# Kernel optimization log

Measured on AMD Instinct MI355X. Metric: run time of the kernel, lower is better.

Reference implementation:

```python
import jax, jax.numpy as jnp
import numpy as np

FFT_SIZE = 1024
HOP = 256

def _dft_weights(fft_size):
    # Matches torch module: np.fft.fft(np.eye(N)) * np.hanning(N)
    # fft_mat[k, n] = exp(-2j*pi*k*n/N) * hanning[n]
    fft_mat = np.fft.fft(np.eye(fft_size)) * np.hanning(fft_size)
    real_w = jnp.asarray(np.real(fft_mat), dtype=jnp.float32)  # [N, N]
    imag_w = jnp.asarray(np.imag(fft_mat), dtype=jnp.float32)  # [N, N]
    return real_w, imag_w

def setup_inputs() -> dict:
    key = jax.random.key(0)
    x = jax.random.normal(key, (32, 160000), dtype=jnp.float32)
    real_w, imag_w = _dft_weights(FFT_SIZE)
    return {"x": x, "real_w": real_w, "imag_w": imag_w}

def reference(x, real_w, imag_w):
    N = FFT_SIZE
    hop = HOP
    B, L = x.shape
    n_frames = (L - N) // hop + 1
    # Frame extraction: frames[b, t, n] = x[b, t*hop + n]
    idx = jnp.arange(n_frames)[:, None] * hop + jnp.arange(N)[None, :]  # [T, N]
    frames = x[:, idx]  # [B, T, N]
    # DFT-as-GEMM (same math as Conv1d(1, N, N, stride=hop) with DFT weights)
    real_x = jnp.einsum('btn,kn->bkt', frames, real_w)  # [B, N, T]
    imag_x = jnp.einsum('btn,kn->bkt', frames, imag_w)  # [B, N, T]
    mag = (real_x ** 2 + imag_x ** 2)[:, :N // 2 + 1, :]  # [B, N//2+1, T]
    phase = jnp.arctan2(imag_x, real_x)  # [B, N, T]
    return (mag, phase)
```

## Files before the change

### kernel.cpp

```cpp
#include <hip/hip_runtime.h>
#include <math.h>

#define NFFT     1024
#define HOP      256
#define NFRAMES  622
#define NBATCH   32
#define XLEN     160000
#define TILE_T   16
#define NPAIR    8
#define ROW      1234
#define KBINS    513
#define NT       512
#define NTILES   39
#define NBLK     (NTILES*NBATCH)

#define PAD(i)   ((i) + 2*((i)>>4) + 4*((i)>>6) + 8*((i)>>8))

#define C1 0.9238795325112867f
#define S1 0.3826834323650898f
#define C2 0.7071067811865476f

__device__ __forceinline__ float2 cmul(float2 a, float2 b) {
    return make_float2(a.x*b.x - a.y*b.y, a.x*b.y + a.y*b.x);
}
__device__ __forceinline__ float2 csqr(float2 a) {
    return make_float2(a.x*a.x - a.y*a.y, 2.0f*a.x*a.y);
}

__device__ __forceinline__ float2 w_of_rev(float f) {
    float s, c;
    asm("v_sin_f32 %0, %1" : "=v"(s) : "v"(f));
    asm("v_cos_f32 %0, %1" : "=v"(c) : "v"(f));
    return make_float2(c, s);
}

__device__ __forceinline__ void bfly4(float2& a, float2& b, float2& c, float2& d,
                                      float2 w1, float2 w2, float2 w3) {
    float2 apc = make_float2(a.x + c.x, a.y + c.y);
    float2 amc = make_float2(a.x - c.x, a.y - c.y);
    float2 bpd = make_float2(b.x + d.x, b.y + d.y);
    float2 bmd = make_float2(b.x - d.x, b.y - d.y);
    float2 y0 = make_float2(apc.x + bpd.x, apc.y + bpd.y);
    float2 y2 = make_float2(apc.x - bpd.x, apc.y - bpd.y);
    float2 y1 = make_float2(amc.x + bmd.y, amc.y - bmd.x);
    float2 y3 = make_float2(amc.x - bmd.y, amc.y + bmd.x);
    a = y0; b = cmul(w1, y1); c = cmul(w2, y2); d = cmul(w3, y3);
}
__device__ __forceinline__ void bfly4_nw(float2& a, float2& b, float2& c, float2& d) {
    float2 apc = make_float2(a.x + c.x, a.y + c.y);
    float2 amc = make_float2(a.x - c.x, a.y - c.y);
    float2 bpd = make_float2(b.x + d.x, b.y + d.y);
    float2 bmd = make_float2(b.x - d.x, b.y - d.y);
    a = make_float2(apc.x + bpd.x, apc.y + bpd.y);
    b = make_float2(amc.x + bmd.y, amc.y - bmd.x);
    c = make_float2(apc.x - bpd.x, apc.y - bpd.y);
    d = make_float2(amc.x - bmd.y, amc.y + bmd.x);
}

__device__ __forceinline__ void fence() {
    asm volatile("s_waitcnt lgkmcnt(0)" ::: "memory");
    __builtin_amdgcn_sched_barrier(0);
}

__device__ __forceinline__ float fast_atan2f(float y, float x) {
    const float ax = fabsf(x), ay = fabsf(y);
    const float mx = fmaxf(ax, ay), mn = fminf(ax, ay);
    float r = mn * __builtin_amdgcn_rcpf(mx);
    if (mx == 0.0f) r = 0.0f;
    const float t = r * r;
    float p = fmaf(t, -0.01172120f, 0.05265332f);
    p = fmaf(t, p, -0.11643287f);
    p = fmaf(t, p, 0.19354346f);
    p = fmaf(t, p, -0.33262347f);
    p = fmaf(t, p, 0.99997726f);
    float a = r * p;
    a = (ay > ax) ? (1.5707963267948966f - a) : a;
    a = (x < 0.0f) ? (3.14159265358979323f - a) : a;
    return copysignf(a, y);
}

__global__ __launch_bounds__(NT, 4)
void spec_kernel(const float* __restrict__ x, const float* __restrict__ win,
                 float* __restrict__ out)
{
    __shared__ __align__(16) float2 zb[NPAIR * ROW];

    const int tid = threadIdx.x;
    const int lg  = (blockIdx.x & 7) * (NBLK / 8) + (blockIdx.x >> 3);
    const int b   = lg / NTILES;
    const int t0  = (lg - b * NTILES) * TILE_T;
    const int wv  = tid >> 6;
    const int ln  = tid & 63;

    {
        const int f0 = t0 + 2*wv, f1 = f0 + 1;
        const float* xb = x + (size_t)b * XLEN;
        const bool v0 = (f0 < NFRAMES), v1 = (f1 < NFRAMES);
        float4* D4 = reinterpret_cast<float4*>(
            &zb[wv*ROW + 4*ln + 2*(ln>>2) + 4*(ln>>4)]);
        #pragma unroll
        for (int q = 0; q < 4; ++q) {
            const int n0 = (q << 8) + (ln << 2);
            const float4 w4 = *reinterpret_cast<const float4*>(&win[n0]);
            float4 a4 = make_float4(0.f, 0.f, 0.f, 0.f), b4 = a4;
            if (v0) a4 = *reinterpret_cast<const float4*>(&xb[f0*HOP + n0]);
            if (v1) b4 = *reinterpret_cast<const float4*>(&xb[f1*HOP + n0]);
            D4[156*q]     = make_float4(w4.x*a4.x, w4.x*b4.x, w4.y*a4.y, w4.y*b4.y);
            D4[156*q + 1] = make_float4(w4.z*a4.z, w4.z*b4.z, w4.w*a4.w, w4.w*b4.w);
        }
    }
    fence();

    {
        float2* p = &zb[wv*ROW + ln + 2*(ln>>4)];
        float2 E[16];
        #pragma unroll
        for (int j = 0; j < 16; ++j) E[j] = p[76*j + 8*(j>>2)];
        const float2 wc = w_of_rev((float)ln * (-1.0f/1024.0f));
        #pragma unroll
        for (int q = 0; q < 4; ++q) {
            float2 w1;
            if      (q == 0) w1 = wc;
            else if (q == 1) w1 = cmul(wc, make_float2(C1, -S1));
            else if (q == 2) w1 = cmul(wc, make_float2(C2, -C2));
            else             w1 = cmul(wc, make_float2(S1, -C1));
            float2 w2 = csqr(w1), w3 = cmul(w1, w2);
            bfly4(E[q], E[q+4], E[q+8], E[q+12], w1, w2, w3);
        }
        const float2 wb  = w_of_rev((float)ln * (-4.0f/1024.0f));
        const float2 wb2 = csqr(wb), wb3 = cmul(wb, wb2);
        #pragma unroll
        for (int u = 0; u < 4; ++u)
            bfly4(E[4*u], E[4*u+1], E[4*u+2], E[4*u+3], wb, wb2, wb3);
        #pragma unroll
        for (int j = 0; j < 16; ++j) p[76*j + 8*(j>>2)] = E[j];
    }
    fence();

    {
        const int m = ln & 15, h = ln >> 4;
        float2* p = &zb[wv*ROW + 76*h + m];
        const float2 w1 = w_of_rev((float)m * (-1.0f/64.0f));
        const float2 w2 = csqr(w1), w3 = cmul(w1, w2);
        #pragma unroll
        for (int u = 0; u < 4; ++u) {
            float2 a  = p[312*u],      bb = p[312*u + 18];
            float2 cc = p[312*u + 36], dd = p[312*u + 54];
            bfly4(a, bb, cc, dd, w1, w2, w3);
            p[312*u]      = a;  p[312*u + 18] = bb;
            p[312*u + 36] = cc; p[312*u + 54] = dd;
        }
    }
    fence();

    {
        float4* p = reinterpret_cast<float4*>(
            &zb[wv*ROW + 18*ln + 4*(ln>>2) + 8*(ln>>4)]);
        float2 F[16];
        #pragma unroll
        for (int r = 0; r < 8; ++r) {
            const float4 v = p[r];
            F[2*r]   = make_float2(v.x, v.y);
            F[2*r+1] = make_float2(v.z, v.w);
        }
        bfly4_nw(F[0], F[4], F[8],  F[12]);
        bfly4(F[1], F[5], F[9],  F[13], make_float2(C1,-S1), make_float2(C2,-C2), make_float2(S1,-C1));
        bfly4(F[2], F[6], F[10], F[14], make_float2(C2,-C2), make_float2(0.f,-1.f), make_float2(-C2,-C2));
        bfly4(F[3], F[7], F[11], F[15], make_float2(S1,-C1), make_float2(-C2,-C2), make_float2(-C1, S1));
        bfly4_nw(F[0],  F[1],  F[2],  F[3]);
        bfly4_nw(F[4],  F[5],  F[6],  F[7]);
        bfly4_nw(F[8],  F[9],  F[10], F[11]);
        bfly4_nw(F[12], F[13], F[14], F[15]);
        #pragma unroll
        for (int r = 0; r < 8; ++r)
            p[r] = make_float4(F[2*r].x, F[2*r].y, F[2*r+1].x, F[2*r+1].y);
    }
    __syncthreads();

    const int kg  = tid >> 3;
    const int jj  = tid & 7;
    const int t_e = t0 + 2*jj;
    const bool tval = (t_e < NFRAMES);

    const int R1 = ((kg & 3) << 8) | ((kg & 12) << 4) | (kg & 48);
    const int km = 64 - kg;
    const int R2 = ((km & 3) << 8) | ((km & 12) << 4) | (km & 48);
    const int J0 = (kg == 0) ? 16 : 15;
    const float2* zp1 = &zb[jj*ROW + PAD(R1)];
    const float2* zp2 = &zb[jj*ROW + PAD(R2)];

    float* magp = out;
    float* php  = out + (size_t)NBATCH * KBINS * NFRAMES;
    const size_t magbase = (size_t)b * KBINS * NFRAMES + t_e;
    const size_t phbase  = (size_t)b * NFFT  * NFRAMES + t_e;

    if (tval) {
        #pragma unroll
        for (int it = 0; it < 9; ++it) {
            if (it == 8 && kg != 0) break;
            const int k  = kg + (it << 6);
            const int c1 = ((it & 3) << 2) | (it >> 2);
            const int j2 = (J0 - it) & 15;
            const int c2 = ((j2 & 3) << 2) | (j2 >> 2);
            const float2 z1 = zp1[c1];
            const float2 z2 = zp2[c2];
            const float re_e = 0.5f*(z1.x + z2.x);
            const float im_e = 0.5f*(z1.y - z2.y);
            const float re_o = 0.5f*(z1.y + z2.y);
            const float im_o = 0.5f*(z2.x - z1.x);
            *reinterpret_cast<float2*>(&magp[magbase + (size_t)k * NFRAMES]) =
                make_float2(fmaf(re_e, re_e, im_e*im_e), fmaf(re_o, re_o, im_o*im_o));
            const float ph_e = fast_atan2f(im_e, re_e);
            const float ph_o = fast_atan2f(im_o, re_o);
            *reinterpret_cast<float2*>(&php[phbase + (size_t)k * NFRAMES]) =
                make_float2(ph_e, ph_o);
            if (k != 0 && k != 512) {
                *reinterpret_cast<float2*>(&php[phbase + (size_t)(NFFT - k) * NFRAMES]) =
                    make_float2(-ph_e, -ph_o);
            }
        }
    }
}

extern "C" void kernel_launch(void* const* d_in, const int* in_sizes, int n_in,
                              void* d_out, int out_size, void* d_ws, size_t ws_size,
                              hipStream_t stream) {
    const float* x  = (const float*)d_in[0];
    const float* rw = (const float*)d_in[1];
    float* out = (float*)d_out;
    spec_kernel<<<dim3(NBLK, 1, 1), dim3(NT, 1, 1), 0, stream>>>(x, rw, out);
}
```

Baseline: 40.27 us.

## Use persistent blocks with atomic tile queue and prefetch next tile's input

```diff
diff --git a/kernel.cpp b/kernel.cpp
--- a/kernel.cpp
+++ b/kernel.cpp
@@ -12,7 +12,8 @@
 #define KBINS    513
 #define NT       512
 #define NTILES   39
-#define NBLK     (NTILES*NBATCH)
+#define NTILES_TOT (NTILES*NBATCH)
+#define NPERSIST 512
 
 #define PAD(i)   ((i) + 2*((i)>>4) + 4*((i)>>6) + 8*((i)>>8))
 
@@ -59,6 +60,12 @@
 
 __device__ __forceinline__ void fence() {
     asm volatile("s_waitcnt lgkmcnt(0)" ::: "memory");
+    __builtin_amdgcn_sched_barrier(0);
+}
+__device__ __forceinline__ void lgk_barrier() {
+    __builtin_amdgcn_sched_barrier(0);
+    asm volatile("s_waitcnt lgkmcnt(0)" ::: "memory");
+    __builtin_amdgcn_s_barrier();
     __builtin_amdgcn_sched_barrier(0);
 }
 
@@ -79,146 +86,193 @@
     return copysignf(a, y);
 }
 
+__device__ __forceinline__ int div39(int v) { return (v * 26887) >> 20; }
+
 __global__ __launch_bounds__(NT, 4)
 void spec_kernel(const float* __restrict__ x, const float* __restrict__ win,
-                 float* __restrict__ out)
+                 float* __restrict__ out, unsigned int* __restrict__ counter)
 {
     __shared__ __align__(16) float2 zb[NPAIR * ROW];
+    __shared__ int sm_next;
 
     const int tid = threadIdx.x;
-    const int lg  = (blockIdx.x & 7) * (NBLK / 8) + (blockIdx.x >> 3);
-    const int b   = lg / NTILES;
-    const int t0  = (lg - b * NTILES) * TILE_T;
     const int wv  = tid >> 6;
     const int ln  = tid & 63;
 
-    {
+    if (tid == 0) sm_next = (int)atomicAdd(counter, 1u);
+    __syncthreads();
+    int tile = sm_next;
+    __syncthreads();
+
+    float4 pa[4], pb[4];
+    if (tile < NTILES_TOT) {
+        const int bb = div39(tile);
+        const int t0 = (tile - bb * NTILES) * TILE_T;
+        const float* xb = x + (size_t)bb * XLEN;
         const int f0 = t0 + 2*wv, f1 = f0 + 1;
-        const float* xb = x + (size_t)b * XLEN;
         const bool v0 = (f0 < NFRAMES), v1 = (f1 < NFRAMES);
-        float4* D4 = reinterpret_cast<float4*>(
-            &zb[wv*ROW + 4*ln + 2*(ln>>2) + 4*(ln>>4)]);
         #pragma unroll
         for (int q = 0; q < 4; ++q) {
             const int n0 = (q << 8) + (ln << 2);
-            const float4 w4 = *reinterpret_cast<const float4*>(&win[n0]);
-            float4 a4 = make_float4(0.f, 0.f, 0.f, 0.f), b4 = a4;
-            if (v0) a4 = *reinterpret_cast<const float4*>(&xb[f0*HOP + n0]);
-            if (v1) b4 = *reinterpret_cast<const float4*>(&xb[f1*HOP + n0]);
-            D4[156*q]     = make_float4(w4.x*a4.x, w4.x*b4.x, w4.y*a4.y, w4.y*b4.y);
-            D4[156*q + 1] = make_float4(w4.z*a4.z, w4.z*b4.z, w4.w*a4.w, w4.w*b4.w);
+            pa[q] = v0 ? *reinterpret_cast<const float4*>(&xb[f0*HOP + n0])
+                       : make_float4(0.f,0.f,0.f,0.f);
+            pb[q] = v1 ? *reinterpret_cast<const float4*>(&xb[f1*HOP + n0])
+                       : make_float4(0.f,0.f,0.f,0.f);
         }
     }
-    fence();
-
-    {
-        float2* p = &zb[wv*ROW + ln + 2*(ln>>4)];
-        float2 E[16];
-        #pragma unroll
-        for (int j = 0; j < 16; ++j) E[j] = p[76*j + 8*(j>>2)];
-        const float2 wc = w_of_rev((float)ln * (-1.0f/1024.0f));
-        #pragma unroll
-        for (int q = 0; q < 4; ++q) {
-            float2 w1;
-            if      (q == 0) w1 = wc;
-            else if (q == 1) w1 = cmul(wc, make_float2(C1, -S1));
-            else if (q == 2) w1 = cmul(wc, make_float2(C2, -C2));
-            else             w1 = cmul(wc, make_float2(S1, -C1));
-            float2 w2 = csqr(w1), w3 = cmul(w1, w2);
-            bfly4(E[q], E[q+4], E[q+8], E[q+12], w1, w2, w3);
-        }
-        const float2 wb  = w_of_rev((float)ln * (-4.0f/1024.0f));
-        const float2 wb2 = csqr(wb), wb3 = cmul(wb, wb2);
-        #pragma unroll
-        for (int u = 0; u < 4; ++u)
-            bfly4(E[4*u], E[4*u+1], E[4*u+2], E[4*u+3], wb, wb2, wb3);
-        #pragma unroll
-        for (int j = 0; j < 16; ++j) p[76*j + 8*(j>>2)] = E[j];
-    }
-    fence();
-
-    {
-        const int m = ln & 15, h = ln >> 4;
-        float2* p = &zb[wv*ROW + 76*h + m];
-        const float2 w1 = w_of_rev((float)m * (-1.0f/64.0f));
-        const float2 w2 = csqr(w1), w3 = cmul(w1, w2);
-        #pragma unroll
-        for (int u = 0; u < 4; ++u) {
-            float2 a  = p[312*u],      bb = p[312*u + 18];
-            float2 cc = p[312*u + 36], dd = p[312*u + 54];
-            bfly4(a, bb, cc, dd, w1, w2, w3);
-            p[312*u]      = a;  p[312*u + 18] = bb;
-            p[312*u + 36] = cc; p[312*u + 54] = dd;
-        }
-    }
-    fence();
-
-    {
-        float4* p = reinterpret_cast<float4*>(
-            &zb[wv*ROW + 18*ln + 4*(ln>>2) + 8*(ln>>4)]);
-        float2 F[16];
-        #pragma unroll
-        for (int r = 0; r < 8; ++r) {
-            const float4 v = p[r];
-            F[2*r]   = make_float2(v.x, v.y);
-            F[2*r+1] = make_float2(v.z, v.w);
-        }
-        bfly4_nw(F[0], F[4], F[8],  F[12]);
-        bfly4(F[1], F[5], F[9],  F[13], make_float2(C1,-S1), make_float2(C2,-C2), make_float2(S1,-C1));
-        bfly4(F[2], F[6], F[10], F[14], make_float2(C2,-C2), make_float2(0.f,-1.f), make_float2(-C2,-C2));
-        bfly4(F[3], F[7], F[11], F[15], make_float2(S1,-C1), make_float2(-C2,-C2), make_float2(-C1, S1));
-        bfly4_nw(F[0],  F[1],  F[2],  F[3]);
-        bfly4_nw(F[4],  F[5],  F[6],  F[7]);
-        bfly4_nw(F[8],  F[9],  F[10], F[11]);
-        bfly4_nw(F[12], F[13], F[14], F[15]);
-        #pragma unroll
-        for (int r = 0; r < 8; ++r)
-            p[r] = make_float4(F[2*r].x, F[2*r].y, F[2*r+1].x, F[2*r+1].y);
-    }
-    __syncthreads();
-
-    const int kg  = tid >> 3;
-    const int jj  = tid & 7;
-    const int t_e = t0 + 2*jj;
-    const bool tval = (t_e < NFRAMES);
-
-    const int R1 = ((kg & 3) << 8) | ((kg & 12) << 4) | (kg & 48);
-    const int km = 64 - kg;
-    const int R2 = ((km & 3) << 8) | ((km & 12) << 4) | (km & 48);
-    const int J0 = (kg == 0) ? 16 : 15;
-    const float2* zp1 = &zb[jj*ROW + PAD(R1)];
-    const float2* zp2 = &zb[jj*ROW + PAD(R2)];
-
-    float* magp = out;
-    float* php  = out + (size_t)NBATCH * KBINS * NFRAMES;
-    const size_t magbase = (size_t)b * KBINS * NFRAMES + t_e;
-    const size_t phbase  = (size_t)b * NFFT  * NFRAMES + t_e;
-
-    if (tval) {
-        #pragma unroll
-        for (int it = 0; it < 9; ++it) {
-            if (it == 8 && kg != 0) break;
-            const int k  = kg + (it << 6);
-            const int c1 = ((it & 3) << 2) | (it >> 2);
-            const int j2 = (J0 - it) & 15;
-            const int c2 = ((j2 & 3) << 2) | (j2 >> 2);
-            const float2 z1 = zp1[c1];
-            const float2 z2 = zp2[c2];
-            const float re_e = 0.5f*(z1.x + z2.x);
-            const float im_e = 0.5f*(z1.y - z2.y);
-            const float re_o = 0.5f*(z1.y + z2.y);
-            const float im_o = 0.5f*(z2.x - z1.x);
-            *reinterpret_cast<float2*>(&magp[magbase + (size_t)k * NFRAMES]) =
-                make_float2(fmaf(re_e, re_e, im_e*im_e), fmaf(re_o, re_o, im_o*im_o));
-            const float ph_e = fast_atan2f(im_e, re_e);
-            const float ph_o = fast_atan2f(im_o, re_o);
-            *reinterpret_cast<float2*>(&php[phbase + (size_t)k * NFRAMES]) =
-                make_float2(ph_e, ph_o);
-            if (k != 0 && k != 512) {
-                *reinterpret_cast<float2*>(&php[phbase + (size_t)(NFFT - k) * NFRAMES]) =
-                    make_float2(-ph_e, -ph_o);
-            }
-        }
+
+    while (tile < NTILES_TOT) {
+        const int bb = div39(tile);
+        const int t0 = (tile - bb * NTILES) * TILE_T;
+
+        {
+            float4* D4 = reinterpret_cast<float4*>(
+                &zb[wv*ROW + 4*ln + 2*(ln>>2) + 4*(ln>>4)]);
+            #pragma unroll
+            for (int q = 0; q < 4; ++q) {
+                const int n0 = (q << 8) + (ln << 2);
+                const float4 w4 = *reinterpret_cast<const float4*>(&win[n0]);
+                D4[156*q]     = make_float4(w4.x*pa[q].x, w4.x*pb[q].x,
+                                            w4.y*pa[q].y, w4.y*pb[q].y);
+                D4[156*q + 1] = make_float4(w4.z*pa[q].z, w4.z*pb[q].z,
+                                            w4.w*pa[q].w, w4.w*pb[q].w);
+            }
+        }
+        fence();
+
+        {
+            float2* p = &zb[wv*ROW + ln + 2*(ln>>4)];
+            float2 E[16];
+            #pragma unroll
+            for (int j = 0; j < 16; ++j) E[j] = p[76*j + 8*(j>>2)];
+            const float2 wc = w_of_rev((float)ln * (-1.0f/1024.0f));
+            #pragma unroll
+            for (int q = 0; q < 4; ++q) {
+                float2 w1;
+                if      (q == 0) w1 = wc;
+                else if (q == 1) w1 = cmul(wc, make_float2(C1, -S1));
+                else if (q == 2) w1 = cmul(wc, make_float2(C2, -C2));
+                else             w1 = cmul(wc, make_float2(S1, -C1));
+                float2 w2 = csqr(w1), w3 = cmul(w1, w2);
+                bfly4(E[q], E[q+4], E[q+8], E[q+12], w1, w2, w3);
+            }
+            const float2 wb  = csqr(csqr(wc));
+            const float2 wb2 = csqr(wb), wb3 = cmul(wb, wb2);
+            #pragma unroll
+            for (int u = 0; u < 4; ++u)
+                bfly4(E[4*u], E[4*u+1], E[4*u+2], E[4*u+3], wb, wb2, wb3);
+            #pragma unroll
+            for (int j = 0; j < 16; ++j) p[76*j + 8*(j>>2)] = E[j];
+        }
+        fence();
+
+        {
+            const int m = ln & 15, h = ln >> 4;
+            float2* p = &zb[wv*ROW + 76*h + m];
+            const float2 w1 = w_of_rev((float)m * (-1.0f/64.0f));
+            const float2 w2 = csqr(w1), w3 = cmul(w1, w2);
+            #pragma unroll
+            for (int u = 0; u < 4; ++u) {
+                float2 a  = p[312*u],      bb2 = p[312*u + 18];
+                float2 cc = p[312*u + 36], dd  = p[312*u + 54];
+                bfly4(a, bb2, cc, dd, w1, w2, w3);
+                p[312*u]      = a;   p[312*u + 18] = bb2;
+                p[312*u + 36] = cc;  p[312*u + 54] = dd;
+            }
+        }
+        fence();
+
+        {
+            float4* p = reinterpret_cast<float4*>(
+                &zb[wv*ROW + 18*ln + 4*(ln>>2) + 8*(ln>>4)]);
+            float2 F[16];
+            #pragma unroll
+            for (int r = 0; r < 8; ++r) {
+                const float4 v = p[r];
+                F[2*r]   = make_float2(v.x, v.y);
+                F[2*r+1] = make_float2(v.z, v.w);
+            }
+            bfly4_nw(F[0], F[4], F[8],  F[12]);
+            bfly4(F[1], F[5], F[9],  F[13], make_float2(C1,-S1), make_float2(C2,-C2), make_float2(S1,-C1));
+            bfly4(F[2], F[6], F[10], F[14], make_float2(C2,-C2), make_float2(0.f,-1.f), make_float2(-C2,-C2));
+            bfly4(F[3], F[7], F[11], F[15], make_float2(S1,-C1), make_float2(-C2,-C2), make_float2(-C1, S1));
+            bfly4_nw(F[0],  F[1],  F[2],  F[3]);
+            bfly4_nw(F[4],  F[5],  F[6],  F[7]);
+            bfly4_nw(F[8],  F[9],  F[10], F[11]);
+            bfly4_nw(F[12], F[13], F[14], F[15]);
+            #pragma unroll
+            for (int r = 0; r < 8; ++r)
+                p[r] = make_float4(F[2*r].x, F[2*r].y, F[2*r+1].x, F[2*r+1].y);
+        }
+
+        if (tid == 0) sm_next = (int)atomicAdd(counter, 1u);
+        lgk_barrier();
+        const int nxt = sm_next;
+
+        if (nxt < NTILES_TOT) {
+            const int nb  = div39(nxt);
+            const int nt0 = (nxt - nb * NTILES) * TILE_T;
+            const float* xb = x + (size_t)nb * XLEN;
+            const int f0 = nt0 + 2*wv, f1 = f0 + 1;
+            const bool v0 = (f0 < NFRAMES), v1 = (f1 < NFRAMES);
+            #pragma unroll
+            for (int q = 0; q < 4; ++q) {
+                const int n0 = (q << 8) + (ln << 2);
+                pa[q] = v0 ? *reinterpret_cast<const float4*>(&xb[f0*HOP + n0])
+                           : make_float4(0.f,0.f,0.f,0.f);
+                pb[q] = v1 ? *reinterpret_cast<const float4*>(&xb[f1*HOP + n0])
+                           : make_float4(0.f,0.f,0.f,0.f);
+            }
+        }
+
+        {
+            const int kg  = tid >> 3;
+            const int jj  = tid & 7;
+            const int t_e = t0 + 2*jj;
+            const bool tval = (t_e < NFRAMES);
+
+            const int R1 = ((kg & 3) << 8) | ((kg & 12) << 4) | (kg & 48);
+            const int km = 64 - kg;
+            const int R2 = ((km & 3) << 8) | ((km & 12) << 4) | (km & 48);
+            const int J0 = (kg == 0) ? 16 : 15;
+            const float2* zp1 = &zb[jj*ROW + PAD(R1)];
+            const float2* zp2 = &zb[jj*ROW + PAD(R2)];
+
+            float* magp = out;
+            float* php  = out + (size_t)NBATCH * KBINS * NFRAMES;
+            const size_t magbase = (size_t)bb * KBINS * NFRAMES + t_e;
+            const size_t phbase  = (size_t)bb * NFFT  * NFRAMES + t_e;
+
+            if (tval) {
+                #pragma unroll
+                for (int it = 0; it < 9; ++it) {
+                    if (it == 8 && kg != 0) break;
+                    const int k  = kg + (it << 6);
+                    const int c1 = ((it & 3) << 2) | (it >> 2);
+                    const int j2 = (J0 - it) & 15;
+                    const int c2 = ((j2 & 3) << 2) | (j2 >> 2);
+                    const float2 z1 = zp1[c1];
+                    const float2 z2 = zp2[c2];
+                    const float re_e = 0.5f*(z1.x + z2.x);
+                    const float im_e = 0.5f*(z1.y - z2.y);
+                    const float re_o = 0.5f*(z1.y + z2.y);
+                    const float im_o = 0.5f*(z2.x - z1.x);
+                    *reinterpret_cast<float2*>(&magp[magbase + (size_t)k * NFRAMES]) =
+                        make_float2(fmaf(re_e, re_e, im_e*im_e),
+                                    fmaf(re_o, re_o, im_o*im_o));
+                    const float ph_e = fast_atan2f(im_e, re_e);
+                    const float ph_o = fast_atan2f(im_o, re_o);
+                    *reinterpret_cast<float2*>(&php[phbase + (size_t)k * NFRAMES]) =
+                        make_float2(ph_e, ph_o);
+                    if (k != 0 && k != 512) {
+                        *reinterpret_cast<float2*>(&php[phbase + (size_t)(NFFT - k) * NFRAMES]) =
+                            make_float2(-ph_e, -ph_o);
+                    }
+                }
+            }
+        }
+        lgk_barrier();
+        tile = nxt;
     }
 }
 
@@ -228,5 +282,7 @@
     const float* x  = (const float*)d_in[0];
     const float* rw = (const float*)d_in[1];
     float* out = (float*)d_out;
-    spec_kernel<<<dim3(NBLK, 1, 1), dim3(NT, 1, 1), 0, stream>>>(x, rw, out);
-}
+    hipMemsetAsync(d_ws, 0, sizeof(unsigned int), stream);
+    spec_kernel<<<dim3(NPERSIST, 1, 1), dim3(NT, 1, 1), 0, stream>>>(
+        x, rw, out, (unsigned int*)d_ws);
+}
```

Result: slower. 98.23 us (+143.9%).
